# Optimization experiments

Hardware: AMD Instinct MI355X
Metric: run time of the kernel (lower is better)

## Reference

```python
import jax, jax.numpy as jnp
import numpy as np

B, N, L = 64, 256, 1024
OUT = L // 2   # ChebConv out_channels = Seq_len / 2
ALPHA = 0.5    # DirGNNConv default alpha


def _glorot(key, shape):
    # PyG ChebConv lins use glorot init
    lim = float(np.sqrt(6.0 / (shape[0] + shape[1])))
    return jax.random.uniform(key, shape, minval=-lim, maxval=lim, dtype=jnp.float32)


def setup_inputs() -> dict:
    key = jax.random.key(0)
    ks = jax.random.split(key, 8)
    x = jax.random.normal(ks[0], (B, N, L), dtype=jnp.float32)
    # dense per-sample adjacency; only used via nonzero() in torch, never enters math (K=1)
    At = jax.random.randint(ks[1], (B, N, N), 0, 2, dtype=jnp.int32)
    W_in = _glorot(ks[2], (L, OUT))
    b_in = jnp.zeros((OUT,), dtype=jnp.float32)
    W_out = _glorot(ks[3], (L, OUT))
    b_out = jnp.zeros((OUT,), dtype=jnp.float32)
    # DirGNNConv root Linear (kaiming-ish uniform; exact init irrelevant for correctness baseline)
    lim = float(1.0 / np.sqrt(L))
    W_root = jax.random.uniform(ks[4], (L, OUT), minval=-lim, maxval=lim, dtype=jnp.float32)
    b_root = jax.random.uniform(ks[5], (OUT,), minval=-lim, maxval=lim, dtype=jnp.float32)
    return {"x": x, "At": At, "W_in": W_in, "b_in": b_in,
            "W_out": W_out, "b_out": b_out, "W_root": W_root, "b_root": b_root}


def reference(x, At, W_in, b_in, W_out, b_out, W_root, b_root):
    # so the batched edge_index built from At.nonzero() never influences the output.
    # DirGNNConv: alpha * conv_out(x) + (1-alpha) * conv_in(x) + root_lin(x).
    xf = x.reshape(B * N, L)                        # [B*N, L]
    y = (ALPHA * (xf @ W_out + b_out)
         + (1.0 - ALPHA) * (xf @ W_in + b_in)
         + (xf @ W_root + b_root))                  # [B*N, OUT]
    return y.reshape(B, N, OUT)
```

## Files before the change

kernel.cpp:

```cpp
#include <hip/hip_runtime.h>
#include <stdint.h>

static constexpr int Mrows = 16384;
static constexpr int Kdim  = 1024;
static constexpr int Ncols = 512;

typedef __attribute__((ext_vector_type(8))) short bf16x8;
typedef __attribute__((ext_vector_type(4))) float f32x4;

__device__ __forceinline__ unsigned short f2bf(float f) {
  unsigned u = __builtin_bit_cast(unsigned, f);
  u += 0x7FFFu + ((u >> 16) & 1u);
  return (unsigned short)(u >> 16);
}
__device__ __forceinline__ unsigned f2bf2(float lo, float hi) {
  unsigned ul = __builtin_bit_cast(unsigned, lo);
  unsigned uh = __builtin_bit_cast(unsigned, hi);
  ul += 0x7FFFu + ((ul >> 16) & 1u);
  uh += 0x7FFFu + ((uh >> 16) & 1u);
  return (ul >> 16) | (uh & 0xFFFF0000u);
}

__device__ __forceinline__ void gl2lds16(const void* g, void* l) {
  __builtin_amdgcn_global_load_lds(
      (const __attribute__((address_space(1))) void*)g,
      (__attribute__((address_space(3))) void*)l, 16, 0, 0);
}

__global__ __launch_bounds__(256) void prep_w(
    const float* __restrict__ Win, const float* __restrict__ Wout,
    const float* __restrict__ Wroot, unsigned short* __restrict__ Wt)
{
  __shared__ unsigned short lds[32 * 36];
  const int t  = threadIdx.x;
  const int b2 = blockIdx.x;
  const int tk0 = (b2 & 31) * 32;
  const int tn0 = (b2 >> 5) * 32;
  {
    const int k  = t >> 3;
    const int nq = (t & 7) * 4;
    const int gi = (tk0 + k) * Ncols + tn0 + nq;
    const float4 wi = *(const float4*)(Win + gi);
    const float4 wo = *(const float4*)(Wout + gi);
    const float4 wr = *(const float4*)(Wroot + gi);
    lds[(nq + 0) * 36 + k] = f2bf(0.5f * (wi.x + wo.x) + wr.x);
    lds[(nq + 1) * 36 + k] = f2bf(0.5f * (wi.y + wo.y) + wr.y);
    lds[(nq + 2) * 36 + k] = f2bf(0.5f * (wi.z + wo.z) + wr.z);
    lds[(nq + 3) * 36 + k] = f2bf(0.5f * (wi.w + wo.w) + wr.w);
  }
  __syncthreads();
  {
    const int n  = t >> 3;
    const int k8 = (t & 7) * 4;
    const ushort4 v = *(const ushort4*)&lds[n * 36 + k8];
    *(ushort4*)(Wt + (size_t)(tn0 + n) * Kdim + tk0 + k8) = v;
  }
}

__global__ __launch_bounds__(256, 2) void gemm_fused(
    const float* __restrict__ x, const unsigned short* __restrict__ Wt,
    const float* __restrict__ b_in, const float* __restrict__ b_out,
    const float* __restrict__ b_root, float* __restrict__ Y)
{
  __shared__ __attribute__((aligned(16))) short As[128 * 32];
  __shared__ __attribute__((aligned(16))) short Bs[128 * 32];

  const int bid = blockIdx.x;
  const int m0 = (bid & 127) * 128;
  const int n0 = (bid >> 7) * 128;

  const int t    = threadIdx.x;
  const int lane = t & 63;
  const int w    = t >> 6;
  const int wm   = w >> 1;
  const int wn   = w & 1;
  const int quad = lane >> 4;
  const int lm   = lane & 15;

  const int sr = lane >> 2;
  const int ss = lane & 3;
  const int sc = ss ^ ((sr >> 1) & 3);
  const float* gX          = x  + (size_t)(m0 + w * 32 + sr) * Kdim + sc * 8;
  const unsigned short* gB = Wt + (size_t)(n0 + w * 32 + sr) * Kdim + sc * 8;
  short* const lA0 = &As[(w * 32 + sr) * 32 + ss * 8];
  short* const lA1 = lA0 + 16 * 32;
  short* const lB0 = &Bs[(w * 32) * 32];
  short* const lB1 = &Bs[(w * 32 + 16) * 32];
  const int rowK = 16 * Kdim;

  const int slot = quad ^ ((lm >> 1) & 3);
  const int aoff = (wm * 64 + lm) * 32 + slot * 8;
  const int boff = (wn * 64 + lm) * 32 + slot * 8;

  f32x4 acc[4][4] = {};

  float4 a00 = *(const float4*)(gX);
  float4 a01 = *(const float4*)(gX + 4);
  float4 a10 = *(const float4*)(gX + rowK);
  float4 a11 = *(const float4*)(gX + rowK + 4);

  #pragma unroll 1
  for (int it = 0; it < 32; ++it) {
    gl2lds16(gB + it * 32,        lB0);
    gl2lds16(gB + it * 32 + rowK, lB1);

    uint4 pa, pb;
    pa.x = f2bf2(a00.x, a00.y); pa.y = f2bf2(a00.z, a00.w);
    pa.z = f2bf2(a01.x, a01.y); pa.w = f2bf2(a01.z, a01.w);
    pb.x = f2bf2(a10.x, a10.y); pb.y = f2bf2(a10.z, a10.w);
    pb.z = f2bf2(a11.x, a11.y); pb.w = f2bf2(a11.z, a11.w);
    *(uint4*)lA0 = pa;
    *(uint4*)lA1 = pb;

    __syncthreads();

    bf16x8 af[4], bfr[4];
    #pragma unroll
    for (int i = 0; i < 4; ++i) af[i]  = *(const bf16x8*)&As[aoff + i * 16 * 32];
    #pragma unroll
    for (int j = 0; j < 4; ++j) bfr[j] = *(const bf16x8*)&Bs[boff + j * 16 * 32];

    if (it < 31) {
      const float* gx = gX + (it + 1) * 32;
      a00 = *(const float4*)(gx);
      a01 = *(const float4*)(gx + 4);
      a10 = *(const float4*)(gx + rowK);
      a11 = *(const float4*)(gx + rowK + 4);
    }

    #pragma unroll
    for (int i = 0; i < 4; ++i)
      #pragma unroll
      for (int j = 0; j < 4; ++j)
        acc[i][j] = __builtin_amdgcn_mfma_f32_16x16x32_bf16(af[i], bfr[j], acc[i][j], 0, 0, 0);

    asm volatile("s_waitcnt lgkmcnt(0)" ::: "memory");
    __builtin_amdgcn_s_barrier();
  }

  #pragma unroll
  for (int j = 0; j < 4; ++j) {
    const int gc = n0 + wn * 64 + j * 16 + lm;
    const float bias = 0.5f * (b_in[gc] + b_out[gc]) + b_root[gc];
    #pragma unroll
    for (int i = 0; i < 4; ++i) {
      const int gr = m0 + wm * 64 + i * 16 + quad * 4;
      float* yp = Y + (size_t)gr * Ncols + gc;
      #pragma unroll
      for (int r = 0; r < 4; ++r)
        yp[(size_t)r * Ncols] = acc[i][j][r] + bias;
    }
  }
}

extern "C" void kernel_launch(void* const* d_in, const int* in_sizes, int n_in,
                              void* d_out, int out_size, void* d_ws, size_t ws_size,
                              hipStream_t stream)
{
  const float* x      = (const float*)d_in[0];
  const float* W_in   = (const float*)d_in[2];
  const float* b_in   = (const float*)d_in[3];
  const float* W_out  = (const float*)d_in[4];
  const float* b_out  = (const float*)d_in[5];
  const float* W_root = (const float*)d_in[6];
  const float* b_root = (const float*)d_in[7];
  float* y = (float*)d_out;

  unsigned short* Wt = (unsigned short*)d_ws;

  prep_w<<<dim3(512), dim3(256), 0, stream>>>(W_in, W_out, W_root, Wt);
  gemm_fused<<<dim3(512), dim3(256), 0, stream>>>(x, Wt, b_in, b_out, b_root, y);
}
```

Measured before the change: 157.9 us.

## Double-buffer LDS tiles and prefetch x two steps ahead in fused GEMM

Doubles the A and B LDS buffers so the next tile's B global-to-LDS loads and the converted A stores overlap with MFMA work on the current tile. Register prefetch of x is deepened to two K-steps using two alternating register sets, and the loop is unrolled by two. A partial vmcnt wait lets later loads stay in flight across the barrier. The cost is double the LDS (32KB per block) and more live registers, which may reduce occupancy at two blocks per CU.

```diff
diff --git a/kernel.cpp b/kernel.cpp
--- a/kernel.cpp
+++ b/kernel.cpp
@@ -62,8 +62,9 @@
     const float* __restrict__ b_in, const float* __restrict__ b_out,
     const float* __restrict__ b_root, float* __restrict__ Y)
 {
-  __shared__ __attribute__((aligned(16))) short As[128 * 32];
-  __shared__ __attribute__((aligned(16))) short Bs[128 * 32];
+  constexpr int BUF = 128 * 32;
+  __shared__ __attribute__((aligned(16))) short As[2 * BUF];
+  __shared__ __attribute__((aligned(16))) short Bs[2 * BUF];
 
   const int bid = blockIdx.x;
   const int m0 = (bid & 127) * 128;
@@ -82,10 +83,9 @@
   const int sc = ss ^ ((sr >> 1) & 3);
   const float* gX          = x  + (size_t)(m0 + w * 32 + sr) * Kdim + sc * 8;
   const unsigned short* gB = Wt + (size_t)(n0 + w * 32 + sr) * Kdim + sc * 8;
-  short* const lA0 = &As[(w * 32 + sr) * 32 + ss * 8];
-  short* const lA1 = lA0 + 16 * 32;
+  short* const lA  = &As[(w * 32 + sr) * 32 + ss * 8];
   short* const lB0 = &Bs[(w * 32) * 32];
-  short* const lB1 = &Bs[(w * 32 + 16) * 32];
+  short* const lB1 = lB0 + 16 * 32;
   const int rowK = 16 * Kdim;
 
   const int slot = quad ^ ((lm >> 1) & 3);
@@ -93,50 +93,84 @@
   const int boff = (wn * 64 + lm) * 32 + slot * 8;
 
   f32x4 acc[4][4] = {};
-
-  float4 a00 = *(const float4*)(gX);
-  float4 a01 = *(const float4*)(gX + 4);
-  float4 a10 = *(const float4*)(gX + rowK);
-  float4 a11 = *(const float4*)(gX + rowK + 4);
+  float4 S0, S1, S2, S3, T0, T1, T2, T3;
+
+#define LOADA(P0, P1, P2, P3, IDX) do {                                   \
+    const float* gx_ = gX + (IDX) * 32;                                   \
+    P0 = *(const float4*)(gx_);                                           \
+    P1 = *(const float4*)(gx_ + 4);                                       \
+    P2 = *(const float4*)(gx_ + rowK);                                    \
+    P3 = *(const float4*)(gx_ + rowK + 4);                                \
+  } while (0)
+
+#define PACKA(P0, P1, P2, P3, NXT) do {                                   \
+    uint4 pa_, pb_;                                                       \
+    pa_.x = f2bf2(P0.x, P0.y); pa_.y = f2bf2(P0.z, P0.w);                 \
+    pa_.z = f2bf2(P1.x, P1.y); pa_.w = f2bf2(P1.z, P1.w);                 \
+    pb_.x = f2bf2(P2.x, P2.y); pb_.y = f2bf2(P2.z, P2.w);                 \
+    pb_.z = f2bf2(P3.x, P3.y); pb_.w = f2bf2(P3.z, P3.w);                 \
+    *(uint4*)(lA + (NXT) * BUF)           = pa_;                          \
+    *(uint4*)(lA + (NXT) * BUF + 16 * 32) = pb_;                          \
+  } while (0)
+
+#define SYNC() do {                                                       \
+    asm volatile("s_waitcnt vmcnt(4) lgkmcnt(0)" ::: "memory");           \
+    __builtin_amdgcn_s_barrier();                                         \
+    __builtin_amdgcn_sched_barrier(0);                                    \
+  } while (0)
+
+#define KSTEP(TT, QA0, QA1, QA2, QA3, RA0, RA1, RA2, RA3) do {            \
+    const int cur_ = (TT) & 1, nxt_ = cur_ ^ 1;                           \
+    gl2lds16(gB + ((TT) + 1) * 32,        lB0 + nxt_ * BUF);              \
+    gl2lds16(gB + ((TT) + 1) * 32 + rowK, lB1 + nxt_ * BUF);              \
+    __builtin_amdgcn_sched_barrier(0);   \
+    bf16x8 af[4], bfr[4];                                                 \
+    _Pragma("unroll") for (int i = 0; i < 4; ++i)                         \
+      af[i]  = *(const bf16x8*)&As[cur_ * BUF + aoff + i * 16 * 32];      \
+    _Pragma("unroll") for (int j = 0; j < 4; ++j)                         \
+      bfr[j] = *(const bf16x8*)&Bs[cur_ * BUF + boff + j * 16 * 32];      \
+    PACKA(QA0, QA1, QA2, QA3, nxt_);                                      \
+    { int ld_ = (TT) + 2; if (ld_ > 31) ld_ = 31;                         \
+      LOADA(RA0, RA1, RA2, RA3, ld_); }                                   \
+    _Pragma("unroll") for (int i = 0; i < 4; ++i)                         \
+      _Pragma("unroll") for (int j = 0; j < 4; ++j)                       \
+        acc[i][j] = __builtin_amdgcn_mfma_f32_16x16x32_bf16(              \
+            af[i], bfr[j], acc[i][j], 0, 0, 0);                           \
+    SYNC();                                                               \
+  } while (0)
+
+  LOADA(S0, S1, S2, S3, 0);
+  gl2lds16(gB, lB0);
+  gl2lds16(gB + rowK, lB1);
+  __builtin_amdgcn_sched_barrier(0);
+  LOADA(T0, T1, T2, T3, 1);
+  PACKA(S0, S1, S2, S3, 0);
+  SYNC();
 
   #pragma unroll 1
-  for (int it = 0; it < 32; ++it) {
-    gl2lds16(gB + it * 32,        lB0);
-    gl2lds16(gB + it * 32 + rowK, lB1);
-
-    uint4 pa, pb;
-    pa.x = f2bf2(a00.x, a00.y); pa.y = f2bf2(a00.z, a00.w);
-    pa.z = f2bf2(a01.x, a01.y); pa.w = f2bf2(a01.z, a01.w);
-    pb.x = f2bf2(a10.x, a10.y); pb.y = f2bf2(a10.z, a10.w);
-    pb.z = f2bf2(a11.x, a11.y); pb.w = f2bf2(a11.z, a11.w);
-    *(uint4*)lA0 = pa;
-    *(uint4*)lA1 = pb;
-
-    __syncthreads();
-
+  for (int it = 0; it < 30; it += 2) {
+    KSTEP(it,     T0, T1, T2, T3, S0, S1, S2, S3);
+    KSTEP(it + 1, S0, S1, S2, S3, T0, T1, T2, T3);
+  }
+  KSTEP(30, T0, T1, T2, T3, S0, S1, S2, S3);
+
+  {
     bf16x8 af[4], bfr[4];
     #pragma unroll
-    for (int i = 0; i < 4; ++i) af[i]  = *(const bf16x8*)&As[aoff + i * 16 * 32];
-    #pragma unroll
-    for (int j = 0; j < 4; ++j) bfr[j] = *(const bf16x8*)&Bs[boff + j * 16 * 32];
-
-    if (it < 31) {
-      const float* gx = gX + (it + 1) * 32;
-      a00 = *(const float4*)(gx);
-      a01 = *(const float4*)(gx + 4);
-      a10 = *(const float4*)(gx + rowK);
-      a11 = *(const float4*)(gx + rowK + 4);
-    }
-
+    for (int i = 0; i < 4; ++i) af[i]  = *(const bf16x8*)&As[BUF + aoff + i * 16 * 32];
+    #pragma unroll
+    for (int j = 0; j < 4; ++j) bfr[j] = *(const bf16x8*)&Bs[BUF + boff + j * 16 * 32];
     #pragma unroll
     for (int i = 0; i < 4; ++i)
       #pragma unroll
       for (int j = 0; j < 4; ++j)
         acc[i][j] = __builtin_amdgcn_mfma_f32_16x16x32_bf16(af[i], bfr[j], acc[i][j], 0, 0, 0);
-
-    asm volatile("s_waitcnt lgkmcnt(0)" ::: "memory");
-    __builtin_amdgcn_s_barrier();
-  }
+  }
+
+#undef KSTEP
+#undef SYNC
+#undef PACKA
+#undef LOADA
 
   #pragma unroll
   for (int j = 0; j < 4; ++j) {
```

After: 159.0 us. About the same (+0.7%).

## Stream fp32 x tiles directly to LDS with multi-stage async pipeline

Applied to the files above, without the earlier changes.

Replaces the register-staged fp32 load and bf16 convert of x with direct global-to-LDS async loads into a triple-buffered fp32 tile. The B operand is double-buffered, and fp32-to-bf16 conversion now happens when fragments are read out of LDS. The tile shape changes from 128x128 to 64x128 with 1024 blocks, an XCD-aware block mapping and higher occupancy (4 blocks per CU). The aim is to overlap memory latency with MFMA work and to take the global loads out of the register path. In exchange, per-block reuse is lower, each row of x is converted once per n-tile, and LDS traffic rises because it now holds fp32 A data.

```diff
diff --git a/kernel.cpp b/kernel.cpp
--- a/kernel.cpp
+++ b/kernel.cpp
@@ -1,12 +1,12 @@
 #include <hip/hip_runtime.h>
 #include <stdint.h>
 
-static constexpr int Mrows = 16384;
 static constexpr int Kdim  = 1024;
 static constexpr int Ncols = 512;
 
 typedef __attribute__((ext_vector_type(8))) short bf16x8;
 typedef __attribute__((ext_vector_type(4))) float f32x4;
+typedef __attribute__((ext_vector_type(4))) unsigned int u32x4;
 
 __device__ __forceinline__ unsigned short f2bf(float f) {
   unsigned u = __builtin_bit_cast(unsigned, f);
@@ -57,99 +57,110 @@
   }
 }
 
-__global__ __launch_bounds__(256, 2) void gemm_fused(
+__global__ __launch_bounds__(256, 4) void gemm_direct(
     const float* __restrict__ x, const unsigned short* __restrict__ Wt,
     const float* __restrict__ b_in, const float* __restrict__ b_out,
     const float* __restrict__ b_root, float* __restrict__ Y)
 {
-  __shared__ __attribute__((aligned(16))) short As[128 * 32];
-  __shared__ __attribute__((aligned(16))) short Bs[128 * 32];
+  __shared__ __attribute__((aligned(16))) float Asf[3][64][32];
+  __shared__ __attribute__((aligned(16))) short Bs[2][128][32];
 
   const int bid = blockIdx.x;
-  const int m0 = (bid & 127) * 128;
-  const int n0 = (bid >> 7) * 128;
+  const int xcd = bid & 7;
+  const int s   = bid >> 3;
+  const int mt  = xcd * 32 + (s >> 2);
+  const int nt  = s & 3;
+  const int m0  = mt * 64;
+  const int n0  = nt * 128;
 
   const int t    = threadIdx.x;
   const int lane = t & 63;
   const int w    = t >> 6;
-  const int wm   = w >> 1;
-  const int wn   = w & 1;
   const int quad = lane >> 4;
   const int lm   = lane & 15;
+
+  const int al  = lane >> 3;
+  const int asl = lane & 7;
+  const int asc = asl ^ al;
+  const float* gA0 = x + (size_t)(m0 + w * 16 + al) * Kdim + asc * 4;
+  const float* gA1 = gA0 + (size_t)8 * Kdim;
 
   const int sr = lane >> 2;
   const int ss = lane & 3;
   const int sc = ss ^ ((sr >> 1) & 3);
-  const float* gX          = x  + (size_t)(m0 + w * 32 + sr) * Kdim + sc * 8;
   const unsigned short* gB = Wt + (size_t)(n0 + w * 32 + sr) * Kdim + sc * 8;
-  short* const lA0 = &As[(w * 32 + sr) * 32 + ss * 8];
-  short* const lA1 = lA0 + 16 * 32;
-  short* const lB0 = &Bs[(w * 32) * 32];
-  short* const lB1 = &Bs[(w * 32 + 16) * 32];
   const int rowK = 16 * Kdim;
 
-  const int slot = quad ^ ((lm >> 1) & 3);
-  const int aoff = (wm * 64 + lm) * 32 + slot * 8;
-  const int boff = (wn * 64 + lm) * 32 + slot * 8;
+  const int a0off = (w * 16 + lm) * 32 + ((2 * quad)     ^ (lm & 7)) * 4;
+  const int a1off = (w * 16 + lm) * 32 + ((2 * quad + 1) ^ (lm & 7)) * 4;
+  const int boff  = lm * 32 + (quad ^ ((lm >> 1) & 3)) * 8;
 
-  f32x4 acc[4][4] = {};
+  f32x4 acc[8] = {};
 
-  float4 a00 = *(const float4*)(gX);
-  float4 a01 = *(const float4*)(gX + 4);
-  float4 a10 = *(const float4*)(gX + rowK);
-  float4 a11 = *(const float4*)(gX + rowK + 4);
+#define STAGE_B(TT, BB) do {                                              \
+    gl2lds16(gB + (TT) * 32,        &Bs[BB][w * 32][0]);                  \
+    gl2lds16(gB + (TT) * 32 + rowK, &Bs[BB][w * 32 + 16][0]);             \
+  } while (0)
+
+#define STAGE_A(TT, AB) do {                                              \
+    gl2lds16(gA0 + (TT) * 32, &Asf[AB][w * 16][0]);                       \
+    gl2lds16(gA1 + (TT) * 32, &Asf[AB][w * 16 + 8][0]);                   \
+  } while (0)
+
+  STAGE_B(0, 0);
+  __builtin_amdgcn_sched_barrier(0);
+  STAGE_A(0, 0);
+  STAGE_A(1, 1);
+  asm volatile("s_waitcnt vmcnt(2)" ::: "memory");
+  __builtin_amdgcn_s_barrier();
+  __builtin_amdgcn_sched_barrier(0);
 
   #pragma unroll 1
   for (int it = 0; it < 32; ++it) {
-    gl2lds16(gB + it * 32,        lB0);
-    gl2lds16(gB + it * 32 + rowK, lB1);
+    const int tb = (it + 1 < 32) ? it + 1 : 31;
+    const int ta = (it + 2 < 32) ? it + 2 : 31;
+    STAGE_B(tb, (it + 1) & 1);
+    __builtin_amdgcn_sched_barrier(0);
+    STAGE_A(ta, (it + 2) % 3);
+    __builtin_amdgcn_sched_barrier(0);
 
-    uint4 pa, pb;
-    pa.x = f2bf2(a00.x, a00.y); pa.y = f2bf2(a00.z, a00.w);
-    pa.z = f2bf2(a01.x, a01.y); pa.w = f2bf2(a01.z, a01.w);
-    pb.x = f2bf2(a10.x, a10.y); pb.y = f2bf2(a10.z, a10.w);
-    pb.z = f2bf2(a11.x, a11.y); pb.w = f2bf2(a11.z, a11.w);
-    *(uint4*)lA0 = pa;
-    *(uint4*)lA1 = pb;
+    const float* ab = &Asf[it % 3][0][0];
+    const f32x4 c0 = *(const f32x4*)(ab + a0off);
+    const f32x4 c1 = *(const f32x4*)(ab + a1off);
+    u32x4 ua;
+    ua.x = f2bf2(c0.x, c0.y); ua.y = f2bf2(c0.z, c0.w);
+    ua.z = f2bf2(c1.x, c1.y); ua.w = f2bf2(c1.z, c1.w);
+    const bf16x8 af = __builtin_bit_cast(bf16x8, ua);
 
-    __syncthreads();
-
-    bf16x8 af[4], bfr[4];
+    const short* bb = &Bs[it & 1][0][0];
+    bf16x8 bfr[8];
     #pragma unroll
-    for (int i = 0; i < 4; ++i) af[i]  = *(const bf16x8*)&As[aoff + i * 16 * 32];
-    #pragma unroll
-    for (int j = 0; j < 4; ++j) bfr[j] = *(const bf16x8*)&Bs[boff + j * 16 * 32];
-
-    if (it < 31) {
-      const float* gx = gX + (it + 1) * 32;
-      a00 = *(const float4*)(gx);
-      a01 = *(const float4*)(gx + 4);
-      a10 = *(const float4*)(gx + rowK);
-      a11 = *(const float4*)(gx + rowK + 4);
-    }
+    for (int j = 0; j < 8; ++j)
+      bfr[j] = *(const bf16x8*)(bb + boff + j * 512);
 
     #pragma unroll
-    for (int i = 0; i < 4; ++i)
-      #pragma unroll
-      for (int j = 0; j < 4; ++j)
-        acc[i][j] = __builtin_amdgcn_mfma_f32_16x16x32_bf16(af[i], bfr[j], acc[i][j], 0, 0, 0);
+    for (int j = 0; j < 8; ++j)
+      acc[j] = __builtin_amdgcn_mfma_f32_16x16x32_bf16(af, bfr[j], acc[j], 0, 0, 0);
 
-    asm volatile("s_waitcnt lgkmcnt(0)" ::: "memory");
+    asm volatile("s_waitcnt vmcnt(2)" ::: "memory");
     __builtin_amdgcn_s_barrier();
+    __builtin_amdgcn_sched_barrier(0);
   }
 
+  asm volatile("s_waitcnt vmcnt(0)" ::: "memory");
+
+#undef STAGE_A
+#undef STAGE_B
+
   #pragma unroll
-  for (int j = 0; j < 4; ++j) {
-    const int gc = n0 + wn * 64 + j * 16 + lm;
+  for (int j = 0; j < 8; ++j) {
+    const int gc = n0 + j * 16 + lm;
     const float bias = 0.5f * (b_in[gc] + b_out[gc]) + b_root[gc];
+    const int gr = m0 + w * 16 + quad * 4;
+    float* yp = Y + (size_t)gr * Ncols + gc;
     #pragma unroll
-    for (int i = 0; i < 4; ++i) {
-      const int gr = m0 + wm * 64 + i * 16 + quad * 4;
-      float* yp = Y + (size_t)gr * Ncols + gc;
-      #pragma unroll
-      for (int r = 0; r < 4; ++r)
-        yp[(size_t)r * Ncols] = acc[i][j][r] + bias;
-    }
+    for (int r = 0; r < 4; ++r)
+      yp[(size_t)r * Ncols] = acc[j][r] + bias;
   }
 }
 
@@ -169,5 +180,5 @@
   unsigned short* Wt = (unsigned short*)d_ws;
 
   prep_w<<<dim3(512), dim3(256), 0, stream>>>(W_in, W_out, W_root, Wt);
-  gemm_fused<<<dim3(512), dim3(256), 0, stream>>>(x, Wt, b_in, b_out, b_root, y);
+  gemm_direct<<<dim3(1024), dim3(256), 0, stream>>>(x, Wt, b_in, b_out, b_root, y);
 }
```

Measured after the change: 166.8 us. 1.06x slower.

## Replace LDS-staged GEMM with direct-to-register loads and double-buffered prefetch

Applied to the files above, without the earlier changes.

Drops shared memory and barriers from the GEMM. Each wave now loads its A (fp32 x, converted to bf16 in registers) and B fragments straight from global memory in MFMA layout, with a two-stage register double buffer. Tiles change to 64 rows by 256 columns per block, so every wave computes a 64x64 sub-tile and the four waves of a block share the same A rows. This removes LDS traffic and synchronisation, but there is no cross-wave reuse through LDS, so each wave re-reads x from global memory/cache, and register pressure rises.

```diff
diff --git a/kernel.cpp b/kernel.cpp
--- a/kernel.cpp
+++ b/kernel.cpp
@@ -1,7 +1,6 @@
 #include <hip/hip_runtime.h>
 #include <stdint.h>
 
-static constexpr int Mrows = 16384;
 static constexpr int Kdim  = 1024;
 static constexpr int Ncols = 512;
 
@@ -20,11 +19,11 @@
   uh += 0x7FFFu + ((uh >> 16) & 1u);
   return (ul >> 16) | (uh & 0xFFFF0000u);
 }
-
-__device__ __forceinline__ void gl2lds16(const void* g, void* l) {
-  __builtin_amdgcn_global_load_lds(
-      (const __attribute__((address_space(1))) void*)g,
-      (__attribute__((address_space(3))) void*)l, 16, 0, 0);
+__device__ __forceinline__ bf16x8 pack8(float4 a, float4 b) {
+  union { unsigned u[4]; bf16x8 v; } r;
+  r.u[0] = f2bf2(a.x, a.y); r.u[1] = f2bf2(a.z, a.w);
+  r.u[2] = f2bf2(b.x, b.y); r.u[3] = f2bf2(b.z, b.w);
+  return r.v;
 }
 
 __global__ __launch_bounds__(256) void prep_w(
@@ -57,94 +56,94 @@
   }
 }
 
-__global__ __launch_bounds__(256, 2) void gemm_fused(
+__global__ __launch_bounds__(256, 2) void gemm_direct(
     const float* __restrict__ x, const unsigned short* __restrict__ Wt,
     const float* __restrict__ b_in, const float* __restrict__ b_out,
     const float* __restrict__ b_root, float* __restrict__ Y)
 {
-  __shared__ __attribute__((aligned(16))) short As[128 * 32];
-  __shared__ __attribute__((aligned(16))) short Bs[128 * 32];
-
-  const int bid = blockIdx.x;
-  const int m0 = (bid & 127) * 128;
-  const int n0 = (bid >> 7) * 128;
+  const int bid   = blockIdx.x;
+  const int panel = bid & 255;
+  const int nhalf = bid >> 8;
+  const int m0    = panel * 64;
 
   const int t    = threadIdx.x;
   const int lane = t & 63;
   const int w    = t >> 6;
-  const int wm   = w >> 1;
-  const int wn   = w & 1;
+  const int n0   = nhalf * 256 + w * 64;
   const int quad = lane >> 4;
   const int lm   = lane & 15;
 
-  const int sr = lane >> 2;
-  const int ss = lane & 3;
-  const int sc = ss ^ ((sr >> 1) & 3);
-  const float* gX          = x  + (size_t)(m0 + w * 32 + sr) * Kdim + sc * 8;
-  const unsigned short* gB = Wt + (size_t)(n0 + w * 32 + sr) * Kdim + sc * 8;
-  short* const lA0 = &As[(w * 32 + sr) * 32 + ss * 8];
-  short* const lA1 = lA0 + 16 * 32;
-  short* const lB0 = &Bs[(w * 32) * 32];
-  short* const lB1 = &Bs[(w * 32 + 16) * 32];
-  const int rowK = 16 * Kdim;
-
-  const int slot = quad ^ ((lm >> 1) & 3);
-  const int aoff = (wm * 64 + lm) * 32 + slot * 8;
-  const int boff = (wn * 64 + lm) * 32 + slot * 8;
+  const float*          gA = x  + (size_t)(m0 + lm) * Kdim + quad * 8;
+  const unsigned short* gB = Wt + (size_t)(n0 + lm) * Kdim + quad * 8;
+  constexpr size_t AROW = (size_t)16 * Kdim;
 
   f32x4 acc[4][4] = {};
 
-  float4 a00 = *(const float4*)(gX);
-  float4 a01 = *(const float4*)(gX + 4);
-  float4 a10 = *(const float4*)(gX + rowK);
-  float4 a11 = *(const float4*)(gX + rowK + 4);
+  float4 PA0a, PA0b, PA1a, PA1b, PA2a, PA2b, PA3a, PA3b;
+  float4 QA0a, QA0b, QA1a, QA1b, QA2a, QA2b, QA3a, QA3b;
+  bf16x8 PB0, PB1, PB2, PB3, QB0, QB1, QB2, QB3;
+
+#define LOADSET(S, KK) do {                                               \
+    const float* a_ = gA + (size_t)(KK) * 32;                             \
+    S##A0a = *(const float4*)(a_);            S##A0b = *(const float4*)(a_ + 4); \
+    S##A1a = *(const float4*)(a_ + AROW);     S##A1b = *(const float4*)(a_ + AROW + 4); \
+    S##A2a = *(const float4*)(a_ + 2 * AROW); S##A2b = *(const float4*)(a_ + 2 * AROW + 4); \
+    S##A3a = *(const float4*)(a_ + 3 * AROW); S##A3b = *(const float4*)(a_ + 3 * AROW + 4); \
+    const unsigned short* b_ = gB + (size_t)(KK) * 32;                    \
+    S##B0 = *(const bf16x8*)(b_);                                         \
+    S##B1 = *(const bf16x8*)(b_ + AROW);                                  \
+    S##B2 = *(const bf16x8*)(b_ + 2 * AROW);                              \
+    S##B3 = *(const bf16x8*)(b_ + 3 * AROW);                              \
+  } while (0)
+
+#define BODY(S, LDKK) do {                                                \
+    bf16x8 af0 = pack8(S##A0a, S##A0b);                                   \
+    bf16x8 af1 = pack8(S##A1a, S##A1b);                                   \
+    bf16x8 af2 = pack8(S##A2a, S##A2b);                                   \
+    bf16x8 af3 = pack8(S##A3a, S##A3b);                                   \
+    bf16x8 bf0 = S##B0, bf1 = S##B1, bf2 = S##B2, bf3 = S##B3;            \
+    if ((LDKK) >= 0) LOADSET(S, LDKK);   \
+    acc[0][0] = __builtin_amdgcn_mfma_f32_16x16x32_bf16(af0, bf0, acc[0][0], 0, 0, 0); \
+    acc[0][1] = __builtin_amdgcn_mfma_f32_16x16x32_bf16(af0, bf1, acc[0][1], 0, 0, 0); \
+    acc[0][2] = __builtin_amdgcn_mfma_f32_16x16x32_bf16(af0, bf2, acc[0][2], 0, 0, 0); \
+    acc[0][3] = __builtin_amdgcn_mfma_f32_16x16x32_bf16(af0, bf3, acc[0][3], 0, 0, 0); \
+    acc[1][0] = __builtin_amdgcn_mfma_f32_16x16x32_bf16(af1, bf0, acc[1][0], 0, 0, 0); \
+    acc[1][1] = __builtin_amdgcn_mfma_f32_16x16x32_bf16(af1, bf1, acc[1][1], 0, 0, 0); \
+    acc[1][2] = __builtin_amdgcn_mfma_f32_16x16x32_bf16(af1, bf2, acc[1][2], 0, 0, 0); \
+    acc[1][3] = __builtin_amdgcn_mfma_f32_16x16x32_bf16(af1, bf3, acc[1][3], 0, 0, 0); \
+    acc[2][0] = __builtin_amdgcn_mfma_f32_16x16x32_bf16(af2, bf0, acc[2][0], 0, 0, 0); \
+    acc[2][1] = __builtin_amdgcn_mfma_f32_16x16x32_bf16(af2, bf1, acc[2][1], 0, 0, 0); \
+    acc[2][2] = __builtin_amdgcn_mfma_f32_16x16x32_bf16(af2, bf2, acc[2][2], 0, 0, 0); \
+    acc[2][3] = __builtin_amdgcn_mfma_f32_16x16x32_bf16(af2, bf3, acc[2][3], 0, 0, 0); \
+    acc[3][0] = __builtin_amdgcn_mfma_f32_16x16x32_bf16(af3, bf0, acc[3][0], 0, 0, 0); \
+    acc[3][1] = __builtin_amdgcn_mfma_f32_16x16x32_bf16(af3, bf1, acc[3][1], 0, 0, 0); \
+    acc[3][2] = __builtin_amdgcn_mfma_f32_16x16x32_bf16(af3, bf2, acc[3][2], 0, 0, 0); \
+    acc[3][3] = __builtin_amdgcn_mfma_f32_16x16x32_bf16(af3, bf3, acc[3][3], 0, 0, 0); \
+  } while (0)
+
+  LOADSET(P, 0);
+  LOADSET(Q, 1);
 
   #pragma unroll 1
-  for (int it = 0; it < 32; ++it) {
-    gl2lds16(gB + it * 32,        lB0);
-    gl2lds16(gB + it * 32 + rowK, lB1);
+  for (int kk = 0; kk < 28; kk += 2) {
+    BODY(P, kk + 2);
+    BODY(Q, kk + 3);
+  }
+  BODY(P, 30);
+  BODY(Q, 31);
+  BODY(P, -1);
+  BODY(Q, -1);
 
-    uint4 pa, pb;
-    pa.x = f2bf2(a00.x, a00.y); pa.y = f2bf2(a00.z, a00.w);
-    pa.z = f2bf2(a01.x, a01.y); pa.w = f2bf2(a01.z, a01.w);
-    pb.x = f2bf2(a10.x, a10.y); pb.y = f2bf2(a10.z, a10.w);
-    pb.z = f2bf2(a11.x, a11.y); pb.w = f2bf2(a11.z, a11.w);
-    *(uint4*)lA0 = pa;
-    *(uint4*)lA1 = pb;
-
-    __syncthreads();
-
-    bf16x8 af[4], bfr[4];
-    #pragma unroll
-    for (int i = 0; i < 4; ++i) af[i]  = *(const bf16x8*)&As[aoff + i * 16 * 32];
-    #pragma unroll
-    for (int j = 0; j < 4; ++j) bfr[j] = *(const bf16x8*)&Bs[boff + j * 16 * 32];
-
-    if (it < 31) {
-      const float* gx = gX + (it + 1) * 32;
-      a00 = *(const float4*)(gx);
-      a01 = *(const float4*)(gx + 4);
-      a10 = *(const float4*)(gx + rowK);
-      a11 = *(const float4*)(gx + rowK + 4);
-    }
-
-    #pragma unroll
-    for (int i = 0; i < 4; ++i)
-      #pragma unroll
-      for (int j = 0; j < 4; ++j)
-        acc[i][j] = __builtin_amdgcn_mfma_f32_16x16x32_bf16(af[i], bfr[j], acc[i][j], 0, 0, 0);
-
-    asm volatile("s_waitcnt lgkmcnt(0)" ::: "memory");
-    __builtin_amdgcn_s_barrier();
-  }
+#undef BODY
+#undef LOADSET
 
   #pragma unroll
   for (int j = 0; j < 4; ++j) {
-    const int gc = n0 + wn * 64 + j * 16 + lm;
+    const int gc = n0 + j * 16 + lm;
     const float bias = 0.5f * (b_in[gc] + b_out[gc]) + b_root[gc];
     #pragma unroll
     for (int i = 0; i < 4; ++i) {
-      const int gr = m0 + wm * 64 + i * 16 + quad * 4;
+      const int gr = m0 + i * 16 + quad * 4;
       float* yp = Y + (size_t)gr * Ncols + gc;
       #pragma unroll
       for (int r = 0; r < 4; ++r)
@@ -169,5 +168,5 @@
   unsigned short* Wt = (unsigned short*)d_ws;
 
   prep_w<<<dim3(512), dim3(256), 0, stream>>>(W_in, W_out, W_root, Wt);
-  gemm_fused<<<dim3(512), dim3(256), 0, stream>>>(x, Wt, b_in, b_out, b_root, y);
+  gemm_direct<<<dim3(512), dim3(256), 0, stream>>>(x, Wt, b_in, b_out, b_root, y);
 }
```

After: 198.6 us. +25.8%, slower.
